# Kernel optimization log

Measured on AMD Instinct MI355X. Metric: run time of the kernel, lower is better.

## Reference

```python
import jax, jax.numpy as jnp
import numpy as np

NUM_SAMPLES = 10
MIN_DIST_PTS = 8
TOP_K = 10
GRID_SIZE = 4
GAP = 0.1


def sample_line_points(seg):
    # seg: [N,2,2] (endpoints, ij coords). Vectorized version of the per-group linspace loop.
    lengths = jnp.linalg.norm(seg[:, 0] - seg[:, 1], axis=1)
    n_samp = jnp.clip(jnp.floor(lengths / MIN_DIST_PTS), 2, NUM_SAMPLES)  # [N]
    t = jnp.arange(NUM_SAMPLES, dtype=seg.dtype)  # [S]
    interval = (seg[:, 1] - seg[:, 0]) / (n_samp[:, None] - 1)  # [N,2]
    pts = seg[:, None, 0, :] + t[None, :, None] * interval[:, None, :]  # [N,S,2]
    valid = t[None, :] < n_samp[:, None]  # [N,S]
    pts = jnp.where(valid[..., None], pts, 0.0)  # original zero-pads invalid samples
    return pts, valid


def grid_sample_norm(desc, pts, img_size):
    # desc: [D,Hc,Wc]; pts: [P,2] (i,j) pixel coords in image of size img_size=(H,W).
    # Replicates kornia normalize_pixel_coordinates + F.grid_sample(align_corners=False,
    # bilinear, zero padding), then L2-normalize along D.
    D, Hc, Wc = desc.shape
    H, W = img_size
    gx = 2.0 * pts[:, 1] / (W - 1) - 1.0
    gy = 2.0 * pts[:, 0] / (H - 1) - 1.0
    ix = ((gx + 1.0) * Wc - 1.0) / 2.0
    iy = ((gy + 1.0) * Hc - 1.0) / 2.0
    x0 = jnp.floor(ix)
    y0 = jnp.floor(iy)
    wx1 = ix - x0
    wy1 = iy - y0
    x0i = x0.astype(jnp.int32)
    y0i = y0.astype(jnp.int32)

    def gather(yi, xi):
        inb = (xi >= 0) & (xi < Wc) & (yi >= 0) & (yi < Hc)
        v = desc[:, jnp.clip(yi, 0, Hc - 1), jnp.clip(xi, 0, Wc - 1)]  # [D,P]
        return v * inb

    v = (gather(y0i, x0i) * (1 - wy1) * (1 - wx1)
         + gather(y0i, x0i + 1) * (1 - wy1) * wx1
         + gather(y0i + 1, x0i) * wy1 * (1 - wx1)
         + gather(y0i + 1, x0i + 1) * wy1 * wx1)
    nrm = jnp.linalg.norm(v, axis=0, keepdims=True)
    return v / jnp.maximum(nrm, 1e-12)


def needleman_wunsch(scores):
    # scores: [B,n,m]. Row-wise scan; the within-row dependency
    # v[j+1]=max(v[j], max(prev[j+1], prev[j]+s)) is a prefix-max (cummax).
    b, n, m = scores.shape
    s = scores - GAP
    init = jnp.zeros((b, m + 1), s.dtype)

    def step(prev, row):  # prev [B,m+1], row [B,m]
        a = jnp.maximum(prev[:, 1:], prev[:, :-1] + row)
        new = jnp.maximum(jax.lax.cummax(a, axis=1), 0.0)
        return jnp.concatenate([jnp.zeros((b, 1), s.dtype), new], axis=1), None

    final, _ = jax.lax.scan(step, init, jnp.swapaxes(s, 0, 1))
    return final[:, -1]


def nw_candidate_scores(scores):
    # scores: [N1,N2,S,S] -> (nw [N1,2k], topk [N1,k])
    ls1 = jnp.max(scores, axis=3)
    v1 = ls1 != -1
    ls1 = jnp.where(v1, ls1, 0.0).sum(2) / v1.sum(2)
    ls2 = jnp.max(scores, axis=2)
    v2 = ls2 != -1
    ls2 = jnp.where(v2, ls2, 0.0).sum(2) / v2.sum(2)
    line_scores = (ls1 + ls2) / 2
    topk = jnp.argsort(line_scores, axis=1)[:, -TOP_K:]  # [N1,k]
    top_scores = jnp.take_along_axis(scores, topk[:, :, None, None], axis=1)  # [N1,k,S,S]
    top_scores = jnp.concatenate([top_scores, jnp.flip(top_scores, axis=-1)], axis=1)  # [N1,2k,S,S]
    N1, t2k, n, m = top_scores.shape
    nw = needleman_wunsch(top_scores.reshape(N1 * t2k, n, m)).reshape(N1, t2k)
    return nw, topk


def filter_and_match(scores):
    nw, topk = nw_candidate_scores(scores)
    t2k = nw.shape[1]
    best = jnp.argmax(nw, axis=1) % (t2k // 2)
    return jnp.take_along_axis(topk, best[:, None], axis=1)[:, 0]


def compute_scores(line_seg1, line_seg2, desc1, desc2):
    S = NUM_SAMPLES
    img1 = (desc1.shape[2] * GRID_SIZE, desc1.shape[3] * GRID_SIZE)
    img2 = (desc2.shape[2] * GRID_SIZE, desc2.shape[3] * GRID_SIZE)
    pts1, val1 = sample_line_points(line_seg1)
    pts2, val2 = sample_line_points(line_seg2)
    d1 = grid_sample_norm(desc1[0], pts1.reshape(-1, 2), img1)  # [D, N1*S]
    d2 = grid_sample_norm(desc2[0], pts2.reshape(-1, 2), img2)  # [D, N2*S]
    sc = d1.T @ d2  # [N1*S, N2*S]
    sc = jnp.where(val1.reshape(-1)[:, None], sc, -1.0)
    sc = jnp.where(val2.reshape(-1)[None, :], sc, -1.0)
    N1, N2 = line_seg1.shape[0], line_seg2.shape[0]
    return sc.reshape(N1, S, N2, S).transpose(0, 2, 1, 3)  # [N1,N2,S,S]


def reference(line_seg1, line_seg2, desc1, desc2):
    scores = compute_scores(line_seg1, line_seg2, desc1, desc2)
    matches = filter_and_match(scores)
    # cross check
    matches2 = filter_and_match(scores.transpose(1, 0, 3, 2))
    mutual = matches2[matches] == jnp.arange(line_seg1.shape[0])
    return jnp.where(mutual, matches, -1).astype(jnp.int32)


def setup_inputs() -> dict:
    key = jax.random.key(0)
    k1, k2, k3, k4 = jax.random.split(key, 4)
    IMG = 512.0
    line_seg1 = jax.random.uniform(k1, (512, 2, 2), dtype=jnp.float32) * (IMG - 1.0)
    line_seg2 = jax.random.uniform(k2, (512, 2, 2), dtype=jnp.float32) * (IMG - 1.0)
    desc1 = jax.random.normal(k3, (1, 128, 128, 128), dtype=jnp.float32)
    desc2 = jax.random.normal(k4, (1, 128, 128, 128), dtype=jnp.float32)
    return {"line_seg1": line_seg1, "line_seg2": line_seg2, "desc1": desc1, "desc2": desc2}
```

## Files before the change

kernel.cpp:

```cpp
#include <hip/hip_runtime.h>
#include <cmath>

#define NL 512
#define SS 10
#define DD 128
#define HWC (128 * 128)

typedef _Float16 f16x8 __attribute__((ext_vector_type(8)));
typedef float f32x4 __attribute__((ext_vector_type(4)));

__device__ __forceinline__ void gload_lds16(const void* g, void* l)
{
    __builtin_amdgcn_global_load_lds(
        (__attribute__((address_space(1))) void*)const_cast<void*>(g),
        (__attribute__((address_space(3))) void*)l, 16, 0, 0);
}

__global__ __launch_bounds__(256) void transpose_kernel(
    const float* __restrict__ in1, const float* __restrict__ in2,
    float* __restrict__ out1, float* __restrict__ out2)
{
    const float* in = blockIdx.z ? in2 : in1;
    float* out = blockIdx.z ? out2 : out1;
    __shared__ float tileT[64 * 65];
    int hw0 = blockIdx.x * 64;
    int d0 = blockIdx.y * 64;
    int tid = threadIdx.x;
#pragma unroll
    for (int p = 0; p < 4; ++p) {
        int f4 = tid + p * 256;
        int row = f4 >> 4;
        int c4 = f4 & 15;
        float4 v = *(const float4*)&in[(size_t)(d0 + row) * HWC + hw0 + c4 * 4];
        tileT[(c4 * 4 + 0) * 65 + row] = v.x;
        tileT[(c4 * 4 + 1) * 65 + row] = v.y;
        tileT[(c4 * 4 + 2) * 65 + row] = v.z;
        tileT[(c4 * 4 + 3) * 65 + row] = v.w;
    }
    __syncthreads();
#pragma unroll
    for (int p = 0; p < 4; ++p) {
        int f4 = tid + p * 256;
        int hw = f4 >> 4;
        int d4 = f4 & 15;
        float4 w;
        w.x = tileT[hw * 65 + d4 * 4 + 0];
        w.y = tileT[hw * 65 + d4 * 4 + 1];
        w.z = tileT[hw * 65 + d4 * 4 + 2];
        w.w = tileT[hw * 65 + d4 * 4 + 3];
        *(float4*)&out[(size_t)(hw0 + hw) * DD + d0 + d4 * 4] = w;
    }
}

__device__ __forceinline__ float fetchd(const float* __restrict__ dt, int y, int x, int d)
{
    bool inb = (x >= 0) && (x < 128) && (y >= 0) && (y < 128);
    int yc = y < 0 ? 0 : (y > 127 ? 127 : y);
    int xc = x < 0 ? 0 : (x > 127 ? 127 : x);
    float v = dt[((size_t)(yc * 128 + xc)) * DD + d];
    return inb ? v : 0.0f;
}

__global__ __launch_bounds__(640) void sample_kernel(
    const float* __restrict__ seg1, const float* __restrict__ seg2,
    const float* __restrict__ dt1, const float* __restrict__ dt2,
    float* __restrict__ dd1, float* __restrict__ dd2,
    _Float16* __restrict__ h1, _Float16* __restrict__ m1,
    _Float16* __restrict__ h2, _Float16* __restrict__ m2,
    int* __restrict__ v1, int* __restrict__ v2)
{
#pragma clang fp contract(off)
    int L = blockIdx.x;
    int img = blockIdx.y;
    const float* seg = img ? seg2 : seg1;
    const float* dt = img ? dt2 : dt1;
    float* dd = img ? dd2 : dd1;
    _Float16* ph = img ? h2 : h1;
    _Float16* pm = img ? m2 : m1;
    int* vv = img ? v2 : v1;

    float p0y = seg[L * 4 + 0], p0x = seg[L * 4 + 1];
    float p1y = seg[L * 4 + 2], p1x = seg[L * 4 + 3];
    float dy = p0y - p1y, dx = p0x - p1x;
    float len = sqrtf(dy * dy + dx * dx);
    float nf = floorf(len / 8.0f);
    nf = fminf(fmaxf(nf, 2.0f), 10.0f);
    int ni = (int)nf;
    float ivy = (p1y - p0y) / (nf - 1.0f);
    float ivx = (p1x - p0x) / (nf - 1.0f);

    int t = threadIdx.x >> 6;
    int lane = threadIdx.x & 63;
    int pt = L * SS + t;
    bool val = t < ni;
    int d0 = lane, d1 = lane + 64;
    float o0 = 0.0f, o1 = 0.0f;
    if (val) {
        float py = p0y + (float)t * ivy;
        float px = p0x + (float)t * ivx;
        float gx = 2.0f * px / 511.0f - 1.0f;
        float gy = 2.0f * py / 511.0f - 1.0f;
        float ix = ((gx + 1.0f) * 128.0f - 1.0f) / 2.0f;
        float iy = ((gy + 1.0f) * 128.0f - 1.0f) / 2.0f;
        float x0f = floorf(ix), y0f = floorf(iy);
        float wx = ix - x0f, wy = iy - y0f;
        int x0 = (int)x0f, y0 = (int)y0f;
        float a00 = fetchd(dt, y0, x0, d0),         b00 = fetchd(dt, y0, x0, d1);
        float a01 = fetchd(dt, y0, x0 + 1, d0),     b01 = fetchd(dt, y0, x0 + 1, d1);
        float a10 = fetchd(dt, y0 + 1, x0, d0),     b10 = fetchd(dt, y0 + 1, x0, d1);
        float a11 = fetchd(dt, y0 + 1, x0 + 1, d0), b11 = fetchd(dt, y0 + 1, x0 + 1, d1);
        float omwx = 1.0f - wx, omwy = 1.0f - wy;
        float va = a00 * omwy * omwx + a01 * omwy * wx + a10 * wy * omwx + a11 * wy * wx;
        float vb = b00 * omwy * omwx + b01 * omwy * wx + b10 * wy * omwx + b11 * wy * wx;
        float s = va * va + vb * vb;
#pragma unroll
        for (int m = 1; m < 64; m <<= 1) s += __shfl_xor(s, m);
        float nrm = sqrtf(s);
        o0 = va / fmaxf(nrm, 1e-12f);
        o1 = vb / fmaxf(nrm, 1e-12f);
    }
    dd[(size_t)pt * DD + d0] = o0;
    dd[(size_t)pt * DD + d1] = o1;
    float xs0 = o0 * 256.0f;
    _Float16 hh0 = (_Float16)xs0;
    _Float16 mm0 = (_Float16)(xs0 - (float)hh0);
    float xs1 = o1 * 256.0f;
    _Float16 hh1 = (_Float16)xs1;
    _Float16 mm1 = (_Float16)(xs1 - (float)hh1);
    int po0 = ((pt >> 4) << 11) + ((d0 >> 3) << 7) + ((pt & 15) << 3) + (d0 & 7);
    int po1 = ((pt >> 4) << 11) + ((d1 >> 3) << 7) + ((pt & 15) << 3) + (d1 & 7);
    ph[po0] = hh0; pm[po0] = mm0;
    ph[po1] = hh1; pm[po1] = mm1;
    if (lane == 0) vv[pt] = val ? 1 : 0;
}

__device__ __forceinline__ void stage_ks(
    const _Float16* __restrict__ ah, const _Float16* __restrict__ am,
    const _Float16* __restrict__ bh, const _Float16* __restrict__ bm,
    int bi, int bj, int ks, int wave, int lane, char* dst)
{
#pragma unroll
    for (int c = 0; c < 10; ++c) {
        int chunk = wave * 10 + c;
        int side = chunk >= 20;
        int rem = side ? chunk - 20 : chunk;
        int plane = rem >= 10;
        int pb = plane ? rem - 10 : rem;
        const _Float16* base = side ? (plane ? bm : bh) : (plane ? am : ah);
        size_t off = ((size_t)((side ? bj : bi) * 10 + pb) << 11) + (ks << 9) + (lane << 3);
        gload_lds16(base + off, dst + (chunk << 10));
    }
}

__global__ __launch_bounds__(256, 2) void gemm_ls_kernel(
    const _Float16* __restrict__ ah_, const _Float16* __restrict__ am_,
    const _Float16* __restrict__ bh_, const _Float16* __restrict__ bm_,
    const int* __restrict__ v1, const int* __restrict__ v2,
    float* __restrict__ ls, float* __restrict__ lsT)
{
    __shared__ __align__(16) char smem[122880];
    int tid = threadIdx.x;
    int wave = tid >> 6, lane = tid & 63;
    int wr = wave >> 1, wc = wave & 1;

    int flat = blockIdx.x;
    int xcd = flat & 7, n = flat >> 3;
    int bi = (xcd >> 1) * 8 + (n >> 4);
    int bj = (xcd & 1) * 16 + (n & 15);

    int fro = ((lane >> 4) << 8) + ((lane & 15) << 4);

    f32x4 zz = {0.0f, 0.0f, 0.0f, 0.0f};
    f32x4 acc[5][5];
#pragma unroll
    for (int i = 0; i < 5; ++i)
#pragma unroll
        for (int j = 0; j < 5; ++j) acc[i][j] = zz;

    stage_ks(ah_, am_, bh_, bm_, bi, bj, 0, wave, lane, smem);
    stage_ks(ah_, am_, bh_, bm_, bi, bj, 1, wave, lane, smem + 40960);

#pragma unroll 1
    for (int ks = 0; ks < 4; ++ks) {
        char* buf = smem + 40960 * (ks % 3);
        if (ks < 2) {
            stage_ks(ah_, am_, bh_, bm_, bi, bj, ks + 2, wave, lane,
                     smem + 40960 * ((ks + 2) % 3));
            asm volatile("s_waitcnt vmcnt(20)" ::: "memory");
        } else if (ks == 2) {
            asm volatile("s_waitcnt vmcnt(10)" ::: "memory");
        } else {
            asm volatile("s_waitcnt vmcnt(0)" ::: "memory");
        }
        __builtin_amdgcn_sched_barrier(0);
        __builtin_amdgcn_s_barrier();
        __builtin_amdgcn_sched_barrier(0);

        f16x8 B0[5], B1[5];
#pragma unroll
        for (int j = 0; j < 5; ++j) {
            int pb = wc * 5 + j;
            B0[j] = *(const f16x8*)(buf + ((20 + pb) << 10) + fro);
            B1[j] = *(const f16x8*)(buf + ((30 + pb) << 10) + fro);
        }
#pragma unroll
        for (int i = 0; i < 5; ++i) {
            int pb = wr * 5 + i;
            f16x8 fh = *(const f16x8*)(buf + (pb << 10) + fro);
            f16x8 fm = *(const f16x8*)(buf + ((10 + pb) << 10) + fro);
#pragma unroll
            for (int j = 0; j < 5; ++j) {
                f32x4 t = acc[i][j];
                t = __builtin_amdgcn_mfma_f32_16x16x32_f16(fh, B0[j], t, 0, 0, 0);
                t = __builtin_amdgcn_mfma_f32_16x16x32_f16(fh, B1[j], t, 0, 0, 0);
                t = __builtin_amdgcn_mfma_f32_16x16x32_f16(fm, B0[j], t, 0, 0, 0);
                acc[i][j] = t;
            }
        }
        __builtin_amdgcn_sched_barrier(0);
        __builtin_amdgcn_s_barrier();
        __builtin_amdgcn_sched_barrier(0);
    }

    float* scr = (float*)smem;
    const float rescale = 1.0f / 65536.0f;
    for (int half = 0; half < 2; ++half) {
        __syncthreads();
        if (wr == half) {
            float* reg = scr + wc * 6464;
#pragma unroll
            for (int i = 0; i < 5; ++i)
#pragma unroll
                for (int j = 0; j < 5; ++j)
#pragma unroll
                    for (int r = 0; r < 4; ++r) {
                        int row = i * 16 + ((lane >> 4) << 2) + r;
                        int col = j * 16 + (lane & 15);
                        int pi = row / 10, s = row - pi * 10;
                        int pj = col / 10, t = col - pj * 10;
                        reg[(pi * 8 + pj) * 101 + s * 10 + t] = acc[i][j][r] * rescale;
                    }
            asm volatile("s_waitcnt lgkmcnt(0)" ::: "memory");
            const float* mp = reg + lane * 101;
            int iL = bi * 16 + half * 8 + (lane >> 3);
            int jL = bj * 16 + wc * 8 + (lane & 7);
            int va[10], vb[10];
#pragma unroll
            for (int s = 0; s < 10; ++s) va[s] = v1[iL * 10 + s];
#pragma unroll
            for (int t = 0; t < 10; ++t) vb[t] = v2[jL * 10 + t];
            float cmx[10];
#pragma unroll
            for (int t = 0; t < 10; ++t) cmx[t] = -3.0e38f;
            float sum1 = 0.0f; int c1 = 0;
#pragma unroll
            for (int s = 0; s < 10; ++s) {
                float rmx = -3.0e38f;
#pragma unroll
                for (int t = 0; t < 10; ++t) {
                    float v = (va[s] && vb[t]) ? mp[s * 10 + t] : -1.0f;
                    rmx = fmaxf(rmx, v);
                    cmx[t] = fmaxf(cmx[t], v);
                }
                if (rmx != -1.0f) { sum1 += rmx; c1++; }
            }
            float sum2 = 0.0f; int c2 = 0;
#pragma unroll
            for (int t = 0; t < 10; ++t) {
                if (cmx[t] != -1.0f) { sum2 += cmx[t]; c2++; }
            }
            float out = (sum1 / (float)c1 + sum2 / (float)c2) * 0.5f;
            ls[(size_t)iL * NL + jL] = out;
            lsT[(size_t)jL * NL + iL] = out;
        }
    }
}

__global__ __launch_bounds__(256) void nw_kernel(
    const float* __restrict__ d1, const float* __restrict__ d2,
    const int* __restrict__ v1, const int* __restrict__ v2,
    const float* __restrict__ ls, const float* __restrict__ lsT,
    int* __restrict__ topkg, float* __restrict__ nwout)
{
    int L = blockIdx.x;
    int dir = blockIdx.y;
    const float* Ad = dir ? d2 : d1;
    const float* Bd = dir ? d1 : d2;
    const int* vA = dir ? v2 : v1;
    const int* vB = dir ? v1 : v2;
    const float* src = dir ? &lsT[(size_t)L * NL] : &ls[(size_t)L * NL];

    __shared__ float Asl[10 * 132];
    __shared__ float Bsl[10][1320];
    __shared__ float M[10][110];
    __shared__ int vam[10], tks[10];

    int tid = threadIdx.x;
    if (tid < 10) vam[tid] = vA[L * 10 + tid];
#pragma unroll
    for (int it = 0; it < 5; ++it) {
        int idx = tid + it * 256;
        int row = idx >> 7, col = idx & 127;
        Asl[row * 132 + col] = Ad[((size_t)L * 10 + row) * DD + col];
    }
    if (tid < 64) {
        int lane = tid;
        float v[8];
#pragma unroll
        for (int it = 0; it < 8; ++it) v[it] = src[it * 64 + lane];
        for (int p = 9; p >= 0; --p) {
            float bv = -3.0e38f;
            int bi_ = -1;
#pragma unroll
            for (int it = 0; it < 8; ++it) {
                int j = it * 64 + lane;
                bool better = (v[it] > bv) || (v[it] == bv && j > bi_);
                if (better) { bv = v[it]; bi_ = j; }
            }
#pragma unroll
            for (int m = 1; m < 64; m <<= 1) {
                float ov = __shfl_xor(bv, m);
                int oi = __shfl_xor(bi_, m);
                bool better = (ov > bv) || (ov == bv && oi > bi_);
                if (better) { bv = ov; bi_ = oi; }
            }
            if ((bi_ & 63) == lane) v[bi_ >> 6] = -3.0e38f;
            if (lane == 0) tks[p] = bi_;
        }
    }
    __syncthreads();
    if (tid < 10) topkg[(size_t)(dir * NL + L) * 10 + tid] = tks[tid];
#pragma unroll
    for (int it = 0; it < 50; ++it) {
        int idx = tid + it * 256;
        int c = idx / 1280;
        int rem = idx - c * 1280;
        int row = rem >> 7, col = rem & 127;
        Bsl[c][row * 132 + col] = Bd[((size_t)tks[c] * 10 + row) * DD + col];
    }
    __syncthreads();
#pragma unroll
    for (int it = 0; it < 4; ++it) {
        int w = tid + it * 256;
        if (w < 1000) {
            int c = w / 100;
            int rem = w - c * 100;
            int s = rem / 10, t = rem - s * 10;
            const float4* ap = (const float4*)&Asl[s * 132];
            const float4* bp = (const float4*)&Bsl[c][t * 132];
            float acc = 0.0f;
#pragma unroll
            for (int k = 0; k < 32; ++k) {
                float4 a = ap[k], b = bp[k];
                acc = fmaf(a.x, b.x, acc);
                acc = fmaf(a.y, b.y, acc);
                acc = fmaf(a.z, b.z, acc);
                acc = fmaf(a.w, b.w, acc);
            }
            int ok = vam[s] && vB[tks[c] * 10 + t];
            M[c][s * 11 + t] = ok ? acc : -1.0f;
        }
    }
    __syncthreads();

    if (tid < 20) {
        int c = tid % 10, f = tid / 10;
        float prev[11];
#pragma unroll
        for (int p = 0; p < 11; ++p) prev[p] = 0.0f;
#pragma unroll
        for (int s = 0; s < 10; ++s) {
            float oldp = prev[0];
            float run = -3.0e38f;
#pragma unroll
            for (int t = 0; t < 10; ++t) {
                int tt = f ? (9 - t) : t;
                float sc = M[c][s * 11 + tt] - 0.1f;
                float pt1 = prev[t + 1];
                float av = fmaxf(pt1, oldp + sc);
                run = fmaxf(run, av);
                prev[t + 1] = fmaxf(run, 0.0f);
                oldp = pt1;
            }
        }
        nwout[((size_t)(dir * NL + L)) * 20 + f * 10 + c] = prev[10];
    }
}

__global__ __launch_bounds__(512) void final_kernel(
    const float* __restrict__ nw, const int* __restrict__ topk, int* __restrict__ out)
{
    __shared__ int m1[NL], m2[NL];
    int t = threadIdx.x;
    {
        const float* p = nw + (size_t)t * 20;
        float bb = -3.0e38f; int kk = 0;
        for (int k = 0; k < 20; ++k) {
            float v = p[k];
            if (v > bb) { bb = v; kk = k; }
        }
        m1[t] = topk[(size_t)t * 10 + (kk % 10)];
    }
    {
        const float* p = nw + (size_t)(NL + t) * 20;
        float bb = -3.0e38f; int kk = 0;
        for (int k = 0; k < 20; ++k) {
            float v = p[k];
            if (v > bb) { bb = v; kk = k; }
        }
        m2[t] = topk[(size_t)(NL + t) * 10 + (kk % 10)];
    }
    __syncthreads();
    int mt = m1[t];
    out[t] = (m2[mt] == t) ? mt : -1;
}

extern "C" void kernel_launch(void* const* d_in, const int* in_sizes, int n_in,
                              void* d_out, int out_size, void* d_ws, size_t ws_size,
                              hipStream_t stream)
{
    const float* seg1 = (const float*)d_in[0];
    const float* seg2 = (const float*)d_in[1];
    const float* desc1 = (const float*)d_in[2];
    const float* desc2 = (const float*)d_in[3];
    int* out = (int*)d_out;

    char* ws = (char*)d_ws;
    size_t off = 0;
    float* dt1 = (float*)(ws + off); off += (size_t)DD * HWC * 4;
    float* dt2 = (float*)(ws + off); off += (size_t)DD * HWC * 4;
    float* dd1 = (float*)(ws + off); off += (size_t)NL * SS * DD * 4;
    float* dd2 = (float*)(ws + off); off += (size_t)NL * SS * DD * 4;
    int* v1 = (int*)(ws + off); off += (size_t)NL * SS * 4;
    int* v2 = (int*)(ws + off); off += (size_t)NL * SS * 4;
    float* ls = (float*)(ws + off); off += (size_t)NL * NL * 4;
    float* lsT = (float*)(ws + off); off += (size_t)NL * NL * 4;
    int* topk = (int*)(ws + off); off += (size_t)2 * NL * 10 * 4;
    float* nwv = (float*)(ws + off); off += (size_t)2 * NL * 20 * 4;
    size_t PL = (size_t)NL * SS * DD;
    _Float16* h1 = (_Float16*)(ws + off); off += PL * 2;
    _Float16* m1 = (_Float16*)(ws + off); off += PL * 2;
    _Float16* h2 = (_Float16*)(ws + off); off += PL * 2;
    _Float16* m2 = (_Float16*)(ws + off); off += PL * 2;

    transpose_kernel<<<dim3(HWC / 64, DD / 64, 2), 256, 0, stream>>>(
        desc1, desc2, dt1, dt2);
    sample_kernel<<<dim3(NL, 2), 640, 0, stream>>>(
        seg1, seg2, dt1, dt2, dd1, dd2, h1, m1, h2, m2, v1, v2);
    gemm_ls_kernel<<<1024, 256, 0, stream>>>(
        h1, m1, h2, m2, v1, v2, ls, lsT);
    nw_kernel<<<dim3(NL, 2), 256, 0, stream>>>(
        dd1, dd2, v1, v2, ls, lsT, topk, nwv);
    final_kernel<<<1, 512, 0, stream>>>(nwv, topk, out);
}
```

Measured before the change: 162.9 us.

## Make GEMM kernel persistent over four tiles with cross-tile load pipelining

The gemm_ls kernel now launches 256 blocks, and each block processes four output tiles in sequence. The triple-buffered k-slice pipeline runs continuously across tile boundaries, so loads for the next tile overlap the epilogue and MFMA work of the current one. The epilogue uses a separate LDS scratch region and is serialized across the four waves. The block's LDS grows to about 145 KB, which likely allows only one block per CU. It also leaves only 256 blocks, so occupancy and parallelism drop in exchange for less pipeline fill and drain per tile.

```diff
diff --git a/kernel.cpp b/kernel.cpp
--- a/kernel.cpp
+++ b/kernel.cpp
@@ -158,15 +158,14 @@
     const int* __restrict__ v1, const int* __restrict__ v2,
     float* __restrict__ ls, float* __restrict__ lsT)
 {
-    __shared__ __align__(16) char smem[122880];
+    __shared__ __align__(16) char smem[148736];
+    float* scr = (float*)(smem + 122880);
     int tid = threadIdx.x;
     int wave = tid >> 6, lane = tid & 63;
     int wr = wave >> 1, wc = wave & 1;
 
-    int flat = blockIdx.x;
-    int xcd = flat & 7, n = flat >> 3;
-    int bi = (xcd >> 1) * 8 + (n >> 4);
-    int bj = (xcd & 1) * 16 + (n & 15);
+    int b = blockIdx.x;
+    int xcd = b & 7, nb = b >> 3;
 
     int fro = ((lane >> 4) << 8) + ((lane & 15) << 4);
 
@@ -177,17 +176,30 @@
 #pragma unroll
         for (int j = 0; j < 5; ++j) acc[i][j] = zz;
 
-    stage_ks(ah_, am_, bh_, bm_, bi, bj, 0, wave, lane, smem);
-    stage_ks(ah_, am_, bh_, bm_, bi, bj, 1, wave, lane, smem + 40960);
-
+#define TILE_BI(n2) ((xcd >> 1) * 8 + ((n2) >> 4))
+#define TILE_BJ(n2) ((xcd & 1) * 16 + ((n2) & 15))
+
+    {
+        int n2 = nb * 4;
+        stage_ks(ah_, am_, bh_, bm_, TILE_BI(n2), TILE_BJ(n2), 0, wave, lane, smem);
+        stage_ks(ah_, am_, bh_, bm_, TILE_BI(n2), TILE_BJ(n2), 1, wave, lane, smem + 40960);
+    }
+
+    const float rescale = 1.0f / 65536.0f;
 #pragma unroll 1
-    for (int ks = 0; ks < 4; ++ks) {
-        char* buf = smem + 40960 * (ks % 3);
-        if (ks < 2) {
-            stage_ks(ah_, am_, bh_, bm_, bi, bj, ks + 2, wave, lane,
-                     smem + 40960 * ((ks + 2) % 3));
+    for (int s = 0; s < 16; ++s) {
+        int q = s >> 2, ks = s & 3;
+        (void)ks;
+        int n2 = nb * 4 + q;
+        int bi = TILE_BI(n2), bj = TILE_BJ(n2);
+
+        if (s < 14) {
+            int s2 = s + 2;
+            int n22 = nb * 4 + (s2 >> 2);
+            stage_ks(ah_, am_, bh_, bm_, TILE_BI(n22), TILE_BJ(n22), s2 & 3,
+                     wave, lane, smem + 40960 * (s2 % 3));
             asm volatile("s_waitcnt vmcnt(20)" ::: "memory");
-        } else if (ks == 2) {
+        } else if (s == 14) {
             asm volatile("s_waitcnt vmcnt(10)" ::: "memory");
         } else {
             asm volatile("s_waitcnt vmcnt(0)" ::: "memory");
@@ -196,6 +208,7 @@
         __builtin_amdgcn_s_barrier();
         __builtin_amdgcn_sched_barrier(0);
 
+        char* buf = smem + 40960 * (s % 3);
         f16x8 B0[5], B1[5];
 #pragma unroll
         for (int j = 0; j < 5; ++j) {
@@ -220,60 +233,67 @@
         __builtin_amdgcn_sched_barrier(0);
         __builtin_amdgcn_s_barrier();
         __builtin_amdgcn_sched_barrier(0);
-    }
-
-    float* scr = (float*)smem;
-    const float rescale = 1.0f / 65536.0f;
-    for (int half = 0; half < 2; ++half) {
-        __syncthreads();
-        if (wr == half) {
-            float* reg = scr + wc * 6464;
+
+        if ((s & 3) == 3) {
+            for (int phz = 0; phz < 4; ++phz) {
+                if (wave == phz) {
+                    float* reg = scr;
+#pragma unroll
+                    for (int i = 0; i < 5; ++i)
+#pragma unroll
+                        for (int j = 0; j < 5; ++j)
+#pragma unroll
+                            for (int r = 0; r < 4; ++r) {
+                                int row = i * 16 + ((lane >> 4) << 2) + r;
+                                int col = j * 16 + (lane & 15);
+                                int pi = row / 10, ss = row - pi * 10;
+                                int pj = col / 10, tt = col - pj * 10;
+                                reg[(pi * 8 + pj) * 101 + ss * 10 + tt] =
+                                    acc[i][j][r] * rescale;
+                            }
+                    asm volatile("s_waitcnt lgkmcnt(0)" ::: "memory");
+                    const float* mp = reg + lane * 101;
+                    int iL = bi * 16 + wr * 8 + (lane >> 3);
+                    int jL = bj * 16 + wc * 8 + (lane & 7);
+                    int va[10], vb[10];
+#pragma unroll
+                    for (int ss = 0; ss < 10; ++ss) va[ss] = v1[iL * 10 + ss];
+#pragma unroll
+                    for (int tt = 0; tt < 10; ++tt) vb[tt] = v2[jL * 10 + tt];
+                    float cmx[10];
+#pragma unroll
+                    for (int tt = 0; tt < 10; ++tt) cmx[tt] = -3.0e38f;
+                    float sum1 = 0.0f; int c1 = 0;
+#pragma unroll
+                    for (int ss = 0; ss < 10; ++ss) {
+                        float rmx = -3.0e38f;
+#pragma unroll
+                        for (int tt = 0; tt < 10; ++tt) {
+                            float v = (va[ss] && vb[tt]) ? mp[ss * 10 + tt] : -1.0f;
+                            rmx = fmaxf(rmx, v);
+                            cmx[tt] = fmaxf(cmx[tt], v);
+                        }
+                        if (rmx != -1.0f) { sum1 += rmx; c1++; }
+                    }
+                    float sum2 = 0.0f; int c2 = 0;
+#pragma unroll
+                    for (int tt = 0; tt < 10; ++tt) {
+                        if (cmx[tt] != -1.0f) { sum2 += cmx[tt]; c2++; }
+                    }
+                    float outv = (sum1 / (float)c1 + sum2 / (float)c2) * 0.5f;
+                    ls[(size_t)iL * NL + jL] = outv;
+                    lsT[(size_t)jL * NL + iL] = outv;
+                }
+                __builtin_amdgcn_s_barrier();
+            }
 #pragma unroll
             for (int i = 0; i < 5; ++i)
 #pragma unroll
-                for (int j = 0; j < 5; ++j)
-#pragma unroll
-                    for (int r = 0; r < 4; ++r) {
-                        int row = i * 16 + ((lane >> 4) << 2) + r;
-                        int col = j * 16 + (lane & 15);
-                        int pi = row / 10, s = row - pi * 10;
-                        int pj = col / 10, t = col - pj * 10;
-                        reg[(pi * 8 + pj) * 101 + s * 10 + t] = acc[i][j][r] * rescale;
-                    }
-            asm volatile("s_waitcnt lgkmcnt(0)" ::: "memory");
-            const float* mp = reg + lane * 101;
-            int iL = bi * 16 + half * 8 + (lane >> 3);
-            int jL = bj * 16 + wc * 8 + (lane & 7);
-            int va[10], vb[10];
-#pragma unroll
-            for (int s = 0; s < 10; ++s) va[s] = v1[iL * 10 + s];
-#pragma unroll
-            for (int t = 0; t < 10; ++t) vb[t] = v2[jL * 10 + t];
-            float cmx[10];
-#pragma unroll
-            for (int t = 0; t < 10; ++t) cmx[t] = -3.0e38f;
-            float sum1 = 0.0f; int c1 = 0;
-#pragma unroll
-            for (int s = 0; s < 10; ++s) {
-                float rmx = -3.0e38f;
-#pragma unroll
-                for (int t = 0; t < 10; ++t) {
-                    float v = (va[s] && vb[t]) ? mp[s * 10 + t] : -1.0f;
-                    rmx = fmaxf(rmx, v);
-                    cmx[t] = fmaxf(cmx[t], v);
-                }
-                if (rmx != -1.0f) { sum1 += rmx; c1++; }
-            }
-            float sum2 = 0.0f; int c2 = 0;
-#pragma unroll
-            for (int t = 0; t < 10; ++t) {
-                if (cmx[t] != -1.0f) { sum2 += cmx[t]; c2++; }
-            }
-            float out = (sum1 / (float)c1 + sum2 / (float)c2) * 0.5f;
-            ls[(size_t)iL * NL + jL] = out;
-            lsT[(size_t)jL * NL + iL] = out;
-        }
-    }
+                for (int j = 0; j < 5; ++j) acc[i][j] = zz;
+        }
+    }
+#undef TILE_BI
+#undef TILE_BJ
 }
 
 __global__ __launch_bounds__(256) void nw_kernel(
@@ -447,7 +467,7 @@
         desc1, desc2, dt1, dt2);
     sample_kernel<<<dim3(NL, 2), 640, 0, stream>>>(
         seg1, seg2, dt1, dt2, dd1, dd2, h1, m1, h2, m2, v1, v2);
-    gemm_ls_kernel<<<1024, 256, 0, stream>>>(
+    gemm_ls_kernel<<<256, 256, 0, stream>>>(
         h1, m1, h2, m2, v1, v2, ls, lsT);
     nw_kernel<<<dim3(NL, 2), 256, 0, stream>>>(
         dd1, dd2, v1, v2, ls, lsT, topk, nwv);
```

Result: slower. 185.4 us (+13.8%).
